# Optimization experiments

Measured on AMD Instinct MI355X. Metric: run time of the kernel, lower is better.

## Reference

```python
import jax, jax.numpy as jnp
import numpy as np

TAU_PRE = 2.0
TAU_POST = 2.0


def setup_inputs() -> dict:
    key = jax.random.key(0)
    k1, k2, k3 = jax.random.split(key, 3)
    T, B, PRE, POST = 64, 16, 4096, 4096
    in_spikes = jax.random.uniform(k1, (T, B, PRE), dtype=jnp.float32)
    out_spikes = jax.random.uniform(k2, (T, B, POST), dtype=jnp.float32)
    weight = jax.random.normal(k3, (POST, PRE), dtype=jnp.float32)
    return {"in_spikes": in_spikes, "out_spikes": out_spikes, "weight": weight}


def reference(in_spikes, out_spikes, weight):
    # in_spikes: [T, B, pre]; out_spikes: [T, B, post]; weight: [post, pre]
    T, B, PRE = in_spikes.shape
    POST = out_spikes.shape[-1]

    def step(carry, xs):
        trace_pre, trace_post, delta_w = carry
        i_sp, o_sp = xs
        trace_pre = jnp.clip(trace_pre - trace_pre / TAU_PRE + i_sp, 0.0, 1.0)  # [B, pre]
        trace_post = trace_post - trace_post / TAU_POST + o_sp  # [B, post]
        # sum_b o[b,post]*trace_pre[b,pre] - (sum_b o[b,post]*trace_post[b,post]) * w[post,pre]
        dw = (jnp.einsum('bo,bp->op', o_sp, trace_pre)
              - (o_sp * trace_post).sum(0)[:, None] * weight)
        return (trace_pre, trace_post, delta_w + dw), None

    init = (jnp.zeros((B, PRE), in_spikes.dtype),
            jnp.zeros((B, POST), out_spikes.dtype),
            jnp.zeros((POST, PRE), weight.dtype))
    (trace_pre, trace_post, delta_w), _ = jax.lax.scan(step, init, (in_spikes, out_spikes))
    return delta_w
```

## Files before the change

### kernel.cpp

```cpp
#include <hip/hip_runtime.h>


#define T_STEPS 64
#define B_SZ    16
#define PRE     4096
#define POST    4096
#define K_TOT   1024

typedef __attribute__((ext_vector_type(8))) unsigned short ushort8;
typedef __attribute__((ext_vector_type(8))) __bf16 bf16x8;
typedef __attribute__((ext_vector_type(4))) float floatx4;

__device__ __forceinline__ unsigned short f2bf(float f) {
    unsigned int u = __float_as_uint(f);
    u += 0x7fff + ((u >> 16) & 1);
    return (unsigned short)(u >> 16);
}

__device__ __forceinline__ void glds16(const void* g, void* l) {
    __builtin_amdgcn_global_load_lds((const __attribute__((address_space(1))) void*)g,
                                     (__attribute__((address_space(3))) void*)l,
                                     16, 0, 0);
}

__global__ __launch_bounds__(256) void trace_convert(
        const float* __restrict__ in_spikes,
        const float* __restrict__ out_spikes,
        unsigned short* __restrict__ AT,
        unsigned short* __restrict__ BT,
        float* __restrict__ coef) {
    __shared__ unsigned short ot[128 * 17];
    __shared__ float cbuf[16 * 17];
    const int tid  = threadIdx.x;
    const bool isA = blockIdx.x >= 256;
    const int p0 = (blockIdx.x & 255) * 16;
    const float* src = isA ? out_spikes : in_spikes;
    unsigned short* dst = isA ? AT : BT;

    const int p = tid & 15;
    const int b = tid >> 4;
    const float* gbase = src + (size_t)b * PRE + p0 + p;

    const int pf = tid >> 4;
    const int ch = tid & 15;
    unsigned short* dstf = &dst[(size_t)(p0 + pf) * K_TOT + ch * 8];

    float x[2][8];
    float st = 0.f, c0 = 0.f;

    #pragma unroll
    for (int tl = 0; tl < 8; ++tl) x[0][tl] = gbase[(size_t)tl * 65536];

    #pragma unroll
    for (int c = 0; c < 8; ++c) {
        if (c < 7) {
            #pragma unroll
            for (int tl = 0; tl < 8; ++tl)
                x[(c + 1) & 1][tl] = gbase[(size_t)((c + 1) * 8 + tl) * 65536];
        }
        #pragma unroll
        for (int tl = 0; tl < 8; ++tl) {
            const float xv = x[c & 1][tl];
            unsigned short ov;
            if (isA) {
                st = 0.5f * st + xv;
                c0 += xv * st;
                ov = f2bf(xv);
            } else {
                st = fminf(fmaxf(0.5f * st + xv, 0.f), 1.f);
                ov = f2bf(st);
            }
            ot[(tl * 16 + b) * 17 + p] = ov;
        }
        asm volatile("s_waitcnt lgkmcnt(0)" ::: "memory");
        __builtin_amdgcn_s_barrier();
        __builtin_amdgcn_sched_barrier(0);

        ushort8 v;
        #pragma unroll
        for (int s = 0; s < 8; ++s) v[s] = ot[(ch * 8 + s) * 17 + pf];
        *(ushort8*)&dstf[c * 128] = v;

        asm volatile("s_waitcnt lgkmcnt(0)" ::: "memory");
        __builtin_amdgcn_s_barrier();
        __builtin_amdgcn_sched_barrier(0);
    }

    if (isA) {
        cbuf[b * 17 + p] = c0;
        asm volatile("s_waitcnt lgkmcnt(0)" ::: "memory");
        __builtin_amdgcn_s_barrier();
        if (tid < 16) {
            float s = 0.f;
            #pragma unroll
            for (int r = 0; r < 16; ++r) s += cbuf[r * 17 + tid];
            coef[p0 + tid] = s;
        }
    }
}

#define BK 64

__global__ __launch_bounds__(256, 2) void stdp_gemm_mfma(
        const unsigned short* __restrict__ AT,
        const unsigned short* __restrict__ BT,
        const float* __restrict__ W,
        const float* __restrict__ coef,
        float* __restrict__ Cout) {
    __shared__ unsigned short As[2][128][BK];
    __shared__ unsigned short Bs[2][128][BK];
    const int tid  = threadIdx.x;
    const int lane = tid & 63;
    const int wave = tid >> 6;
    const int wm = (wave >> 1) * 64;
    const int wn = (wave & 1) * 64;

    const int bid = blockIdx.x;
    const int f   = (bid & 7) * 128 + (bid >> 3);
    const int m0  = (f >> 5) * 128;
    const int n0  = (f & 31) * 128;

    floatx4 acc[4][4];
    #pragma unroll
    for (int i = 0; i < 4; ++i)
        #pragma unroll
        for (int j = 0; j < 4; ++j)
            acc[i][j] = (floatx4){0.f, 0.f, 0.f, 0.f};

    const int srow = tid >> 3;
    const int qg   = (tid & 7) ^ (srow & 7);
    const unsigned short* ga = &AT[(size_t)(m0 + srow) * K_TOT + qg * 8];
    const unsigned short* gb = &BT[(size_t)(n0 + srow) * K_TOT + qg * 8];

    const int rm = lane & 15;
    const int q  = lane >> 4;
    const int sw = rm & 7;

    #define STAGE(t, buf)                                                      \
        do {                                                                   \
            char* laB_ = (char*)&As[buf][0][0] + wave * 1024;                  \
            char* lbB_ = (char*)&Bs[buf][0][0] + wave * 1024;                  \
            const unsigned short* ga_ = ga + (t) * BK;                         \
            const unsigned short* gb_ = gb + (t) * BK;                         \
            _Pragma("unroll")                                                  \
            for (int i_ = 0; i_ < 4; ++i_) {                                   \
                glds16(ga_ + (size_t)i_ * 32 * K_TOT, laB_ + i_ * 4096);       \
                glds16(gb_ + (size_t)i_ * 32 * K_TOT, lbB_ + i_ * 4096);       \
            }                                                                  \
        } while (0)

    STAGE(0, 0);
    __syncthreads();

    #pragma unroll
    for (int t = 0; t < K_TOT / BK; ++t) {
        const int buf = t & 1;
        if (t + 1 < K_TOT / BK) STAGE(t + 1, buf ^ 1);
        #pragma unroll
        for (int h = 0; h < 2; ++h) {
            const int ks = ((h * 4 + q) ^ sw) * 8;
            bf16x8 af[4], bv[4];
            #pragma unroll
            for (int i = 0; i < 4; ++i) {
                af[i] = *(const bf16x8*)&As[buf][wm + i * 16 + rm][ks];
                bv[i] = *(const bf16x8*)&Bs[buf][wn + i * 16 + rm][ks];
            }
            __builtin_amdgcn_s_setprio(1);
            #pragma unroll
            for (int mi = 0; mi < 4; ++mi)
                #pragma unroll
                for (int ni = 0; ni < 4; ++ni)
                    acc[mi][ni] = __builtin_amdgcn_mfma_f32_16x16x32_bf16(
                        af[mi], bv[ni], acc[mi][ni], 0, 0, 0);
            __builtin_amdgcn_s_setprio(0);
        }
        __syncthreads();
    }
    #undef STAGE

    const int colp = n0 + wn + rm;
    const int rowb = m0 + wm + (lane >> 4) * 4;
    #pragma unroll
    for (int mi = 0; mi < 4; ++mi) {
        #pragma unroll
        for (int r = 0; r < 4; ++r) {
            const int o = rowb + mi * 16 + r;
            const float cf = coef[o];
            const float* wr = &W[(size_t)o * PRE];
            float* cr = &Cout[(size_t)o * PRE];
            #pragma unroll
            for (int ni = 0; ni < 4; ++ni) {
                const int p = colp + ni * 16;
                const float wv = __builtin_nontemporal_load(&wr[p]);
                __builtin_nontemporal_store(acc[mi][ni][r] - cf * wv, &cr[p]);
            }
        }
    }
}

extern "C" void kernel_launch(void* const* d_in, const int* in_sizes, int n_in,
                              void* d_out, int out_size, void* d_ws, size_t ws_size,
                              hipStream_t stream) {
    const float* in_spikes  = (const float*)d_in[0];
    const float* out_spikes = (const float*)d_in[1];
    const float* weight     = (const float*)d_in[2];
    float* out = (float*)d_out;

    unsigned short* AT = (unsigned short*)d_ws;
    unsigned short* BT = AT + (size_t)POST * K_TOT;
    float* coef = (float*)(BT + (size_t)PRE * K_TOT);

    trace_convert<<<512, 256, 0, stream>>>(in_spikes, out_spikes, AT, BT, coef);

    stdp_gemm_mfma<<<1024, 256, 0, stream>>>(AT, BT, weight, coef, out);
}
```

Baseline: 186.4 us.

## Pre-swizzle operands into MFMA fragment layout and load directly to registers

The conversion kernel now writes A and B in a tiled layout that matches the MFMA 16x16x32 fragment order, so each lane's 8 bf16 values sit contiguously per 16-row tile and k-block. The GEMM drops LDS staging, barriers and the global_load_lds path, and instead loads fragments from global memory straight into registers, double-buffering them in registers across k-blocks. This removes LDS traffic and synchronisation, but the two waves sharing an A tile (and the two sharing a B tile) now each fetch it separately from L2/global with no LDS sharing. The extra register buffers and the dropped occupancy hint may also lower occupancy.

```diff
diff --git a/kernel.cpp b/kernel.cpp
--- a/kernel.cpp
+++ b/kernel.cpp
@@ -17,17 +17,11 @@
     return (unsigned short)(u >> 16);
 }
 
-__device__ __forceinline__ void glds16(const void* g, void* l) {
-    __builtin_amdgcn_global_load_lds((const __attribute__((address_space(1))) void*)g,
-                                     (__attribute__((address_space(3))) void*)l,
-                                     16, 0, 0);
-}
-
 __global__ __launch_bounds__(256) void trace_convert(
         const float* __restrict__ in_spikes,
         const float* __restrict__ out_spikes,
-        unsigned short* __restrict__ AT,
-        unsigned short* __restrict__ BT,
+        unsigned short* __restrict__ FA,
+        unsigned short* __restrict__ FB,
         float* __restrict__ coef) {
     __shared__ unsigned short ot[128 * 17];
     __shared__ float cbuf[16 * 17];
@@ -35,15 +29,17 @@
     const bool isA = blockIdx.x >= 256;
     const int p0 = (blockIdx.x & 255) * 16;
     const float* src = isA ? out_spikes : in_spikes;
-    unsigned short* dst = isA ? AT : BT;
+    unsigned short* dst = isA ? FA : FB;
 
     const int p = tid & 15;
     const int b = tid >> 4;
     const float* gbase = src + (size_t)b * PRE + p0 + p;
 
-    const int pf = tid >> 4;
-    const int ch = tid & 15;
-    unsigned short* dstf = &dst[(size_t)(p0 + pf) * K_TOT + ch * 8];
+    const int kbl = tid >> 6;
+    const int l   = tid & 63;
+    const int lq  = l >> 4;
+    const int lr  = l & 15;
+    unsigned short* dstf = dst + (size_t)(p0 >> 4) * 16384 + kbl * 512 + l * 8;
 
     float x[2][8];
     float st = 0.f, c0 = 0.f;
@@ -78,8 +74,9 @@
 
         ushort8 v;
         #pragma unroll
-        for (int s = 0; s < 8; ++s) v[s] = ot[(ch * 8 + s) * 17 + pf];
-        *(ushort8*)&dstf[c * 128] = v;
+        for (int s = 0; s < 8; ++s)
+            v[s] = ot[(kbl * 32 + lq * 8 + s) * 17 + lr];
+        *(ushort8*)&dstf[(size_t)c * 2048] = v;
 
         asm volatile("s_waitcnt lgkmcnt(0)" ::: "memory");
         __builtin_amdgcn_s_barrier();
@@ -99,26 +96,23 @@
     }
 }
 
-#define BK 64
-
-__global__ __launch_bounds__(256, 2) void stdp_gemm_mfma(
-        const unsigned short* __restrict__ AT,
-        const unsigned short* __restrict__ BT,
+__global__ __launch_bounds__(256) void stdp_gemm_mfma(
+        const unsigned short* __restrict__ FA,
+        const unsigned short* __restrict__ FB,
         const float* __restrict__ W,
         const float* __restrict__ coef,
         float* __restrict__ Cout) {
-    __shared__ unsigned short As[2][128][BK];
-    __shared__ unsigned short Bs[2][128][BK];
     const int tid  = threadIdx.x;
     const int lane = tid & 63;
     const int wave = tid >> 6;
-    const int wm = (wave >> 1) * 64;
-    const int wn = (wave & 1) * 64;
 
     const int bid = blockIdx.x;
     const int f   = (bid & 7) * 128 + (bid >> 3);
-    const int m0  = (f >> 5) * 128;
-    const int n0  = (f & 31) * 128;
+    const int mt0 = (f >> 5) * 8;
+    const int nt0 = (f & 31) * 8;
+
+    const int wmt = (wave >> 1) * 4;
+    const int wnt = (wave & 1) * 4;
 
     floatx4 acc[4][4];
     #pragma unroll
@@ -127,59 +121,49 @@
         for (int j = 0; j < 4; ++j)
             acc[i][j] = (floatx4){0.f, 0.f, 0.f, 0.f};
 
-    const int srow = tid >> 3;
-    const int qg   = (tid & 7) ^ (srow & 7);
-    const unsigned short* ga = &AT[(size_t)(m0 + srow) * K_TOT + qg * 8];
-    const unsigned short* gb = &BT[(size_t)(n0 + srow) * K_TOT + qg * 8];
-
-    const int rm = lane & 15;
-    const int q  = lane >> 4;
-    const int sw = rm & 7;
-
-    #define STAGE(t, buf)                                                      \
+    const unsigned short* pa[4];
+    const unsigned short* pb[4];
+    #pragma unroll
+    for (int i = 0; i < 4; ++i) {
+        pa[i] = FA + (size_t)(mt0 + wmt + i) * 16384 + lane * 8;
+        pb[i] = FB + (size_t)(nt0 + wnt + i) * 16384 + lane * 8;
+    }
+
+    #define LOADSET(AA, BB, kb)                                                \
         do {                                                                   \
-            char* laB_ = (char*)&As[buf][0][0] + wave * 1024;                  \
-            char* lbB_ = (char*)&Bs[buf][0][0] + wave * 1024;                  \
-            const unsigned short* ga_ = ga + (t) * BK;                         \
-            const unsigned short* gb_ = gb + (t) * BK;                         \
             _Pragma("unroll")                                                  \
             for (int i_ = 0; i_ < 4; ++i_) {                                   \
-                glds16(ga_ + (size_t)i_ * 32 * K_TOT, laB_ + i_ * 4096);       \
-                glds16(gb_ + (size_t)i_ * 32 * K_TOT, lbB_ + i_ * 4096);       \
+                AA[i_] = *(const bf16x8*)(pa[i_] + (size_t)(kb) * 512);        \
+                BB[i_] = *(const bf16x8*)(pb[i_] + (size_t)(kb) * 512);        \
             }                                                                  \
         } while (0)
 
-    STAGE(0, 0);
-    __syncthreads();
-
-    #pragma unroll
-    for (int t = 0; t < K_TOT / BK; ++t) {
-        const int buf = t & 1;
-        if (t + 1 < K_TOT / BK) STAGE(t + 1, buf ^ 1);
-        #pragma unroll
-        for (int h = 0; h < 2; ++h) {
-            const int ks = ((h * 4 + q) ^ sw) * 8;
-            bf16x8 af[4], bv[4];
-            #pragma unroll
-            for (int i = 0; i < 4; ++i) {
-                af[i] = *(const bf16x8*)&As[buf][wm + i * 16 + rm][ks];
-                bv[i] = *(const bf16x8*)&Bs[buf][wn + i * 16 + rm][ks];
-            }
-            __builtin_amdgcn_s_setprio(1);
-            #pragma unroll
-            for (int mi = 0; mi < 4; ++mi)
-                #pragma unroll
-                for (int ni = 0; ni < 4; ++ni)
-                    acc[mi][ni] = __builtin_amdgcn_mfma_f32_16x16x32_bf16(
-                        af[mi], bv[ni], acc[mi][ni], 0, 0, 0);
-            __builtin_amdgcn_s_setprio(0);
-        }
-        __syncthreads();
-    }
-    #undef STAGE
-
-    const int colp = n0 + wn + rm;
-    const int rowb = m0 + wm + (lane >> 4) * 4;
+    #define MFMASET(AA, BB)                                                    \
+        do {                                                                   \
+            _Pragma("unroll")                                                  \
+            for (int mi = 0; mi < 4; ++mi)                                     \
+                _Pragma("unroll")                                              \
+                for (int ni = 0; ni < 4; ++ni)                                 \
+                    acc[mi][ni] = __builtin_amdgcn_mfma_f32_16x16x32_bf16(     \
+                        AA[mi], BB[ni], acc[mi][ni], 0, 0, 0);                 \
+        } while (0)
+
+    bf16x8 a0[4], b0[4], a1[4], b1[4];
+    LOADSET(a0, b0, 0);
+    #pragma unroll 4
+    for (int kb2 = 0; kb2 < 16; ++kb2) {
+        const int k1 = 2 * kb2 + 1;
+        const int k2 = (2 * kb2 + 2) & 31;
+        LOADSET(a1, b1, k1);
+        MFMASET(a0, b0);
+        LOADSET(a0, b0, k2);
+        MFMASET(a1, b1);
+    }
+    #undef LOADSET
+    #undef MFMASET
+
+    const int colp = (nt0 + wnt) * 16 + (lane & 15);
+    const int rowb = (mt0 + wmt) * 16 + (lane >> 4) * 4;
     #pragma unroll
     for (int mi = 0; mi < 4; ++mi) {
         #pragma unroll
@@ -206,11 +190,11 @@
     const float* weight     = (const float*)d_in[2];
     float* out = (float*)d_out;
 
-    unsigned short* AT = (unsigned short*)d_ws;
-    unsigned short* BT = AT + (size_t)POST * K_TOT;
-    float* coef = (float*)(BT + (size_t)PRE * K_TOT);
-
-    trace_convert<<<512, 256, 0, stream>>>(in_spikes, out_spikes, AT, BT, coef);
-
-    stdp_gemm_mfma<<<1024, 256, 0, stream>>>(AT, BT, weight, coef, out);
-}
+    unsigned short* FA = (unsigned short*)d_ws;
+    unsigned short* FB = FA + (size_t)POST * K_TOT;
+    float* coef = (float*)(FB + (size_t)PRE * K_TOT);
+
+    trace_convert<<<512, 256, 0, stream>>>(in_spikes, out_spikes, FA, FB, coef);
+
+    stdp_gemm_mfma<<<1024, 256, 0, stream>>>(FA, FB, weight, coef, out);
+}
```

After: 197.6 us. 6.0% more time.
